# Performance work log

Measured on AMD Instinct MI355X. Metric: run time of the kernel, lower is better.

## Reference

```python
import jax, jax.numpy as jnp
import numpy as np

B, L, E, H = 1, 4096, 1024, 16
D = E // H
EPS = 1e-6


def setup_inputs() -> dict:
    key = jax.random.key(0)
    k1, k2, k3 = jax.random.split(key, 3)
    # fan-in scaled init to keep activations sane
    x = jax.random.normal(k1, (B, L, E), dtype=jnp.float32)
    qkv_w = jax.random.normal(k2, (E, 3 * E), dtype=jnp.float32) / np.sqrt(E)
    qkv_b = jnp.zeros((3 * E,), dtype=jnp.float32)
    out_w = jax.random.normal(k3, (E, E), dtype=jnp.float32) / np.sqrt(E)
    out_b = jnp.zeros((E,), dtype=jnp.float32)
    return {"x": x, "qkv_w": qkv_w, "qkv_b": qkv_b, "out_w": out_w, "out_b": out_b}


def reference(x, qkv_w, qkv_b, out_w, out_b):
    b, l, e = x.shape
    qkv = x @ qkv_w + qkv_b                      # (B, L, 3E)
    q, k, v = jnp.split(qkv, 3, axis=-1)
    # (B, L, E) -> (B, H, L, D)
    q = q.reshape(b, l, H, D).transpose(0, 2, 1, 3)
    k = k.reshape(b, l, H, D).transpose(0, 2, 1, 3)
    v = v.reshape(b, l, H, D).transpose(0, 2, 1, 3)
    q_prime = jax.nn.elu(q) + 1.0
    k_prime = jax.nn.elu(k) + 1.0
    # cumulative sum of per-position outer products k'_l v_l^T : (B,H,L,D,D)
    kv_prod = jnp.einsum('bhld,bhle->bhlde', k_prime, v)
    kv_cumsum = jnp.cumsum(kv_prod, axis=2)
    context = jnp.einsum('bhld,bhlde->bhle', q_prime, kv_cumsum)  # (B,H,L,D)
    k_cumsum = jnp.cumsum(k_prime, axis=2)                        # (B,H,L,D)
    norm = jnp.einsum('bhld,bhld->bhl', q_prime, k_cumsum)        # (B,H,L)
    output = context / (norm[..., None] + EPS)
    output = output.transpose(0, 2, 1, 3).reshape(b, l, e)
    return output @ out_w + out_b
```

## Files before the change

### kernel.cpp

```cpp
#include <hip/hip_runtime.h>
#include <cstddef>
#include <cstdint>

#define L_SEQ 4096
#define EMB   1024
#define NH    16
#define HD    64
#define N3    3072
#define CHUNK 64
#define NCHUNK 64
#define EPS 1e-6f

typedef __attribute__((ext_vector_type(8))) short   bf16x8;
typedef __attribute__((ext_vector_type(4))) short   bf16x4;
typedef __attribute__((ext_vector_type(4))) float   floatx4;

#define AS1 __attribute__((address_space(1)))
#define AS3 __attribute__((address_space(3)))

__device__ __forceinline__ void gload_lds16(const void* g, void* l) {
    __builtin_amdgcn_global_load_lds((AS1 const unsigned int*)g,
                                     (AS3 unsigned int*)l, 16, 0, 0);
}

__device__ __forceinline__ short f2bf(float f) {
    union { float f; unsigned u; } a; a.f = f;
    unsigned r = a.u + 0x7fffu + ((a.u >> 16) & 1u);
    return (short)(r >> 16);
}
__device__ __forceinline__ float bf2f(short s) {
    union { unsigned u; float f; } a; a.u = ((unsigned)(unsigned short)s) << 16;
    return a.f;
}

__device__ __forceinline__ void transpose_tile(const float* __restrict__ W,
                                               short* __restrict__ WT,
                                               int K, int N, int bx, int by,
                                               float (*t)[65], int tid)
{
    const int r  = tid >> 4;
    const int c4 = (tid & 15) << 2;
#pragma unroll
    for (int s = 0; s < 4; ++s) {
        const int k = r + s * 16;
        const floatx4 v = *(const floatx4*)&W[(size_t)(by * 64 + k) * N + bx * 64 + c4];
        t[k][c4 + 0] = v[0]; t[k][c4 + 1] = v[1];
        t[k][c4 + 2] = v[2]; t[k][c4 + 3] = v[3];
    }
    __syncthreads();
#pragma unroll
    for (int s = 0; s < 4; ++s) {
        const int n = r + s * 16;
        bf16x4 o;
        o[0] = f2bf(t[c4 + 0][n]); o[1] = f2bf(t[c4 + 1][n]);
        o[2] = f2bf(t[c4 + 2][n]); o[3] = f2bf(t[c4 + 3][n]);
        *(bf16x4*)&WT[(size_t)(bx * 64 + n) * K + by * 64 + c4] = o;
    }
}

__global__ __launch_bounds__(256)
void prep(const float* __restrict__ x, short* __restrict__ xb,
          const float* __restrict__ qkv_w, short* __restrict__ qwt,
          const float* __restrict__ out_w, short* __restrict__ owt)
{
    __shared__ float t[64][65];
    const int b = blockIdx.x;
    const int tid = threadIdx.x;
    if (b < 2048) {
        const int i = b * 256 + tid;
        const floatx4 a = *(const floatx4*)(x + (size_t)i * 8);
        const floatx4 c = *(const floatx4*)(x + (size_t)i * 8 + 4);
        bf16x8 o;
        o[0] = f2bf(a[0]); o[1] = f2bf(a[1]); o[2] = f2bf(a[2]); o[3] = f2bf(a[3]);
        o[4] = f2bf(c[0]); o[5] = f2bf(c[1]); o[6] = f2bf(c[2]); o[7] = f2bf(c[3]);
        *(bf16x8*)(xb + (size_t)i * 8) = o;
    } else if (b < 2048 + 768) {
        const int u = b - 2048;
        transpose_tile(qkv_w, qwt, EMB, N3, u % 48, u / 48, t, tid);
    } else {
        const int u = b - 2816;
        transpose_tile(out_w, owt, EMB, EMB, u & 15, u >> 4, t, tid);
    }
}

#define MFMA16 __builtin_amdgcn_mfma_f32_16x16x32_bf16

__global__ __launch_bounds__(512, 2)
void mfma_gemm_qkv256(const short* __restrict__ A, const short* __restrict__ BT,
                      const float* __restrict__ bias,
                      short* __restrict__ OQ, short* __restrict__ OK,
                      short* __restrict__ OV)
{
    __shared__ __align__(16) short lds[65536];
    const int tid  = threadIdx.x;
    const int lane = tid & 63;
    const int wave = tid >> 6;
    const int wr   = wave >> 2;
    const int wc   = wave & 3;
    const int frow = lane & 15;
    const int quad = lane >> 4;
    const int q8   = quad * 8;
    const int bx = blockIdx.x;
    const int by = blockIdx.y;

    const short* Ab = A  + (size_t)(by * 256) * 1024;
    const short* Bb = BT + (size_t)(bx * 256) * 1024;

    const int trow = tid >> 3;
    const int ccol = (tid & 7) * 8;
    const int scol = ccol ^ ((trow & 12) << 2);
    const int sx = (frow & 12) << 2;
    const int wcb = wc * 64 + frow;

#define STG(LBASE, GPTR) do {                                               \
        const short* g_ = (GPTR);                                           \
        _Pragma("unroll")                                                   \
        for (int j_ = 0; j_ < 2; ++j_) {                                    \
            const int r_ = j_ * 64 + trow;                                  \
            gload_lds16(g_ + (size_t)r_ * 1024 + scol,                      \
                        &lds[(LBASE) + r_ * 64 + ccol]);                    \
        }                                                                   \
    } while (0)

#define LDA(BASE, R, KS) \
    (*(const bf16x8*)&lds[(BASE) + (R) * 64 + ((((KS) * 32) + q8) ^ sx)])

    floatx4 acc[8][4] = {};
    bf16x8  bq[4][2];

#define PHASE(ABASE, BBASE, QD, RDB, VM, ...) do {                          \
        const int Rr_ = wr * 128 + (QD) * 32 + frow;                        \
        bf16x8 a0_ = LDA((ABASE), Rr_,      0);                             \
        bf16x8 a1_ = LDA((ABASE), Rr_,      1);                             \
        bf16x8 a2_ = LDA((ABASE), Rr_ + 16, 0);                             \
        bf16x8 a3_ = LDA((ABASE), Rr_ + 16, 1);                             \
        if (RDB) {                                                          \
            _Pragma("unroll")                                               \
            for (int ni_ = 0; ni_ < 4; ++ni_) {                             \
                bq[ni_][0] = LDA((BBASE), wcb + ni_ * 16, 0);               \
                bq[ni_][1] = LDA((BBASE), wcb + ni_ * 16, 1);               \
            }                                                               \
        }                                                                   \
        __VA_ARGS__;                                                        \
        __builtin_amdgcn_sched_barrier(0);                                  \
        __builtin_amdgcn_s_barrier();                                       \
        asm volatile("s_waitcnt lgkmcnt(0)" ::: "memory");                  \
        __builtin_amdgcn_sched_barrier(0);                                  \
        __builtin_amdgcn_s_setprio(1);                                      \
        _Pragma("unroll")                                                   \
        for (int ni_ = 0; ni_ < 4; ++ni_) {                                 \
            acc[2*(QD)  ][ni_] = MFMA16(a0_, bq[ni_][0], acc[2*(QD)  ][ni_], 0,0,0); \
            acc[2*(QD)  ][ni_] = MFMA16(a1_, bq[ni_][1], acc[2*(QD)  ][ni_], 0,0,0); \
            acc[2*(QD)+1][ni_] = MFMA16(a2_, bq[ni_][0], acc[2*(QD)+1][ni_], 0,0,0); \
            acc[2*(QD)+1][ni_] = MFMA16(a3_, bq[ni_][1], acc[2*(QD)+1][ni_], 0,0,0); \
        }                                                                   \
        __builtin_amdgcn_s_setprio(0);                                      \
        if (VM) asm volatile("s_waitcnt vmcnt(4)" ::: "memory");            \
        __builtin_amdgcn_s_barrier();                                       \
        __builtin_amdgcn_sched_barrier(0);                                  \
    } while (0)

    STG(0,     Ab);
    STG(8192,  Ab + 131072);
    STG(16384, Bb);
    STG(24576, Bb + 131072);
    STG(49152, Bb + 64);
    STG(57344, Bb + 131072 + 64);
    asm volatile("s_waitcnt vmcnt(4)" ::: "memory");
    __builtin_amdgcn_s_barrier();
    __builtin_amdgcn_sched_barrier(0);

#pragma unroll 1
    for (int it = 0; it < 8; ++it) {
        const int k1  = (2 * it + 1) * 64;
        const int kn0 = ((2 * it + 2) & 15) * 64;
        const int kn1 = ((2 * it + 3) & 15) * 64;

        PHASE(0, 16384, 0, 1, 0,
              STG(32768, Ab + k1); STG(40960, Ab + 131072 + k1));
        PHASE(0, 16384, 1, 0, 0, STG(16384, Bb + kn0));
        PHASE(0, 16384, 2, 0, 0, STG(24576, Bb + 131072 + kn0));
        PHASE(0, 16384, 3, 0, 1, ((void)0));
        PHASE(32768, 49152, 0, 1, 0, STG(0,    Ab + kn0));
        PHASE(32768, 49152, 1, 0, 0, STG(8192, Ab + 131072 + kn0));
        PHASE(32768, 49152, 2, 0, 0, STG(49152, Bb + kn1));
        PHASE(32768, 49152, 3, 0, 1, STG(57344, Bb + 131072 + kn1));
    }

    __syncthreads();

    const int wbase = wave * 8192;
    const int colg0 = bx * 256 + wc * 64;
    const int rsel  = colg0 >> 10;
    const bool do_elu = rsel < 2;
    short* obase = (rsel == 0) ? OQ : (rsel == 1 ? OK : OV);
    const int h  = (colg0 >> 6) & 15;
    const int L0 = by * 256 + wr * 128;
#pragma unroll
    for (int ni = 0; ni < 4; ++ni) {
        const float bv = bias[colg0 + ni * 16 + frow];
#pragma unroll
        for (int mi = 0; mi < 8; ++mi)
#pragma unroll
            for (int r = 0; r < 4; ++r) {
                float v = acc[mi][ni][r] + bv;
                if (do_elu) v = (v > 0.f) ? (v + 1.f) : __expf(v);
                lds[wbase + (mi * 16 + quad * 4 + r) * 64 + ni * 16 + frow] = f2bf(v);
            }
    }
#pragma unroll
    for (int s = 0; s < 16; ++s) {
        const int chunk = s * 64 + lane;
        const int row = chunk >> 3, c8 = (chunk & 7) * 8;
        *(bf16x8*)&obase[((size_t)(h * L_SEQ + L0 + row)) * HD + c8] =
            *(const bf16x8*)&lds[wbase + row * 64 + c8];
    }
#undef PHASE
#undef LDA
#undef STG
}

__global__ __launch_bounds__(256)
void mfma_gemm_out(const short* __restrict__ A, const short* __restrict__ BT,
                   const float* __restrict__ bias, float* __restrict__ OF,
                   int N, int K)
{
    __shared__ __align__(16) short smem[12288];
    short* pan[4] = { smem, smem + 2048, smem + 6144, smem + 8192 };
    const int tid  = threadIdx.x;
    const int lane = tid & 63;
    const int wave = tid >> 6;
    const int wm = (wave >> 1) * 32;
    const int wn = (wave & 1) * 64;
    const int bx = blockIdx.x;
    const int by = blockIdx.y;
    const int frow = lane & 15;
    const int quad = lane >> 4;
    const int fko  = quad << 3;

    const short* Ab = A  + (size_t)(by * 64) * K;
    const short* Bb = BT + (size_t)(bx * 128) * K;

    floatx4 acc[2][4] = {};

    for (int k0 = 0; k0 < K; k0 += 64) {
#pragma unroll
        for (int p = 0; p < 2; ++p) {
            const int kp = k0 + p * 32;
            {
                const int row = tid >> 2;
                const int kc  = (tid & 3) << 3;
                gload_lds16(Ab + (size_t)row * K + kp + kc, &pan[p * 2 + 0][tid << 3]);
            }
#pragma unroll
            for (int q = 0; q < 2; ++q) {
                const int ib = q * 256 + tid;
                const int row = ib >> 2;
                const int kc  = (ib & 3) << 3;
                gload_lds16(Bb + (size_t)row * K + kp + kc, &pan[p * 2 + 1][ib << 3]);
            }
        }
        __syncthreads();
#pragma unroll
        for (int p = 0; p < 2; ++p) {
            bf16x8 af[2], bfv[4];
#pragma unroll
            for (int mi = 0; mi < 2; ++mi)
                af[mi] = *(const bf16x8*)&pan[p * 2 + 0][(wm + mi * 16 + frow) * 32 + fko];
#pragma unroll
            for (int ni = 0; ni < 4; ++ni)
                bfv[ni] = *(const bf16x8*)&pan[p * 2 + 1][(wn + ni * 16 + frow) * 32 + fko];
#pragma unroll
            for (int mi = 0; mi < 2; ++mi)
#pragma unroll
                for (int ni = 0; ni < 4; ++ni)
                    acc[mi][ni] = __builtin_amdgcn_mfma_f32_16x16x32_bf16(
                        af[mi], bfv[ni], acc[mi][ni], 0, 0, 0);
        }
        __syncthreads();
    }

    const int rq = quad << 2;
#pragma unroll
    for (int ni = 0; ni < 4; ++ni) {
        const int n = bx * 128 + wn + ni * 16 + frow;
        const float bv = bias[n];
#pragma unroll
        for (int mi = 0; mi < 2; ++mi)
#pragma unroll
            for (int r = 0; r < 4; ++r) {
                const int m = by * 64 + wm + mi * 16 + rq + r;
                OF[(size_t)m * N + n] = acc[mi][ni][r] + bv;
            }
    }
}

#define SP 72

__global__ __launch_bounds__(256, 4)
void chunk_state(const short* __restrict__ Kb, const short* __restrict__ Vb,
                 short* __restrict__ ScTb, float* __restrict__ zc)
{
    __shared__ __align__(16) short Vt[64 * SP];
    __shared__ __align__(16) short Kt[64 * SP];
    const int c = blockIdx.x, h = blockIdx.y;
    const int tid = threadIdx.x, lane = tid & 63, wave = tid >> 6;
    const int frow = lane & 15;
    const int quad = lane >> 4;
    const int fko  = quad << 3;
    const int wm   = wave << 4;
    const short* Kg = Kb + ((size_t)h * L_SEQ + (size_t)c * CHUNK) * HD;
    const short* Vg = Vb + ((size_t)h * L_SEQ + (size_t)c * CHUNK) * HD;

#pragma unroll
    for (int q = 0; q < 2; ++q) {
        const int idx = q * 256 + tid;
        const int l = idx >> 3, c8 = (idx & 7) << 3;
        const bf16x8 vv = *(const bf16x8*)&Vg[l * 64 + c8];
        const bf16x8 kk = *(const bf16x8*)&Kg[l * 64 + c8];
#pragma unroll
        for (int j = 0; j < 8; ++j) {
            Vt[(c8 + j) * SP + l] = vv[j];
            Kt[(c8 + j) * SP + l] = kk[j];
        }
    }
    __syncthreads();

    const bf16x8 af0 = *(const bf16x8*)&Vt[(wm + frow) * SP + fko];
    const bf16x8 af1 = *(const bf16x8*)&Vt[(wm + frow) * SP + 32 + fko];

    floatx4 acc[4] = {};
#pragma unroll
    for (int n = 0; n < 4; ++n) {
        const bf16x8 kf0 = *(const bf16x8*)&Kt[(n * 16 + frow) * SP + fko];
        const bf16x8 kf1 = *(const bf16x8*)&Kt[(n * 16 + frow) * SP + 32 + fko];
        acc[n] = __builtin_amdgcn_mfma_f32_16x16x32_bf16(af0, kf0, acc[n], 0, 0, 0);
        acc[n] = __builtin_amdgcn_mfma_f32_16x16x32_bf16(af1, kf1, acc[n], 0, 0, 0);
    }

    short* Sout = ScTb + (size_t)(h * NCHUNK + c) * 4096;
#pragma unroll
    for (int n = 0; n < 4; ++n)
#pragma unroll
        for (int r = 0; r < 4; ++r) {
            const int e = wm + quad * 4 + r;
            const int d = n * 16 + frow;
            Sout[e * 64 + d] = f2bf(acc[n][r]);
        }

    if (wave == 0) {
        bf16x8 ones;
#pragma unroll
        for (int j = 0; j < 8; ++j) ones[j] = (short)0x3F80;
        floatx4 zacc[4] = {};
#pragma unroll
        for (int n = 0; n < 4; ++n) {
            const bf16x8 kf0 = *(const bf16x8*)&Kt[(n * 16 + frow) * SP + fko];
            const bf16x8 kf1 = *(const bf16x8*)&Kt[(n * 16 + frow) * SP + 32 + fko];
            zacc[n] = __builtin_amdgcn_mfma_f32_16x16x32_bf16(ones, kf0, zacc[n], 0, 0, 0);
            zacc[n] = __builtin_amdgcn_mfma_f32_16x16x32_bf16(ones, kf1, zacc[n], 0, 0, 0);
        }
        if (quad == 0) {
#pragma unroll
            for (int n = 0; n < 4; ++n)
                zc[(size_t)(h * NCHUNK + c) * 64 + n * 16 + frow] = zacc[n][0];
        }
    }
}

__global__ __launch_bounds__(256)
void prefix_scan(const short* __restrict__ ScTb, const float* __restrict__ zc,
                 short* __restrict__ S0b)
{
    const int g = blockIdx.x * 256 + threadIdx.x;
    const int h  = g >> 12;
    const int ed = g & 4095;
    const int e  = ed >> 6;
    const int d  = ed & 63;
    const short* src = ScTb + (size_t)h * NCHUNK * 4096 + ed;
    float run = 0.f;
    for (int cb = 0; cb < NCHUNK; cb += 8) {
        short v[8];
#pragma unroll
        for (int u = 0; u < 8; ++u) v[u] = src[(size_t)(cb + u) * 4096];
#pragma unroll
        for (int u = 0; u < 8; ++u) {
            S0b[((size_t)((h * NCHUNK + cb + u) * 65 + e)) * 64 + d] = f2bf(run);
            run += bf2f(v[u]);
        }
    }
    if (g < NH * HD) {
        const int h2 = g >> 6, d2 = g & 63;
        float rz = 0.f;
        for (int cb = 0; cb < NCHUNK; cb += 8) {
            float w[8];
#pragma unroll
            for (int u = 0; u < 8; ++u)
                w[u] = zc[((size_t)(h2 * NCHUNK + cb + u)) * HD + d2];
#pragma unroll
            for (int u = 0; u < 8; ++u) {
                S0b[((size_t)((h2 * NCHUNK + cb + u) * 65 + 64)) * 64 + d2] = f2bf(rz);
                rz += w[u];
            }
        }
    }
}

__global__ __launch_bounds__(256)
void chunk_attn(const short* __restrict__ Qb, const short* __restrict__ Kb,
                const short* __restrict__ Vb, const short* __restrict__ S0b,
                short* __restrict__ attn)
{
    __shared__ __align__(16) short Vs[65 * SP];
    __shared__ __align__(16) short As[64 * SP];
    const int c = blockIdx.x, h = blockIdx.y;
    const int tid = threadIdx.x, lane = tid & 63, wave = tid >> 6;
    const size_t rb = ((size_t)h * L_SEQ + (size_t)c * CHUNK) * HD;
    const short* Qg = Qb + rb;
    const short* Kg = Kb + rb;
    const short* Vg = Vb + rb;
    const short* Sg = S0b + (size_t)(h * NCHUNK + c) * 65 * 64;

#pragma unroll
    for (int q = 0; q < 2; ++q) {
        const int idx = q * 256 + tid;
        const int row = idx >> 3, c8 = (idx & 7) << 3;
        const bf16x8 vv = *(const bf16x8*)&Vg[row * 64 + c8];
#pragma unroll
        for (int j = 0; j < 8; ++j) Vs[(c8 + j) * SP + row] = vv[j];
    }
    if (tid < 64) Vs[64 * SP + tid] = (short)0x3F80;
    __syncthreads();

    const int frow = lane & 15;
    const int quad = lane >> 4;
    const int fko  = quad << 3;
    const int wm   = wave << 4;

    const bf16x8 qf0 = *(const bf16x8*)&Qg[(wm + frow) * 64 + fko];
    const bf16x8 qf1 = *(const bf16x8*)&Qg[(wm + frow) * 64 + 32 + fko];

    floatx4 sacc[4] = {};
#pragma unroll
    for (int n = 0; n < 4; ++n) {
        const bf16x8 kf0 = *(const bf16x8*)&Kg[(n * 16 + frow) * 64 + fko];
        const bf16x8 kf1 = *(const bf16x8*)&Kg[(n * 16 + frow) * 64 + 32 + fko];
        sacc[n] = __builtin_amdgcn_mfma_f32_16x16x32_bf16(qf0, kf0, sacc[n], 0, 0, 0);
        sacc[n] = __builtin_amdgcn_mfma_f32_16x16x32_bf16(qf1, kf1, sacc[n], 0, 0, 0);
    }
#pragma unroll
    for (int n = 0; n < 4; ++n)
#pragma unroll
        for (int r = 0; r < 4; ++r) {
            const int i = wm + quad * 4 + r;
            const int j = n * 16 + frow;
            As[i * SP + j] = (j <= i) ? f2bf(sacc[n][r]) : (short)0;
        }
    const bf16x8 af0 = *(const bf16x8*)&As[(wm + frow) * SP + fko];
    const bf16x8 af1 = *(const bf16x8*)&As[(wm + frow) * SP + 32 + fko];

    floatx4 oacc[5] = {};
#pragma unroll
    for (int n = 0; n < 4; ++n) {
        const bf16x8 vf0 = *(const bf16x8*)&Vs[(n * 16 + frow) * SP + fko];
        const bf16x8 vf1 = *(const bf16x8*)&Vs[(n * 16 + frow) * SP + 32 + fko];
        oacc[n] = __builtin_amdgcn_mfma_f32_16x16x32_bf16(af0, vf0, oacc[n], 0, 0, 0);
        oacc[n] = __builtin_amdgcn_mfma_f32_16x16x32_bf16(af1, vf1, oacc[n], 0, 0, 0);
        const bf16x8 sf0 = *(const bf16x8*)&Sg[(n * 16 + frow) * 64 + fko];
        const bf16x8 sf1 = *(const bf16x8*)&Sg[(n * 16 + frow) * 64 + 32 + fko];
        oacc[n] = __builtin_amdgcn_mfma_f32_16x16x32_bf16(qf0, sf0, oacc[n], 0, 0, 0);
        oacc[n] = __builtin_amdgcn_mfma_f32_16x16x32_bf16(qf1, sf1, oacc[n], 0, 0, 0);
    }
    {
        const bf16x8 vf0 = *(const bf16x8*)&Vs[64 * SP + fko];
        const bf16x8 vf1 = *(const bf16x8*)&Vs[64 * SP + 32 + fko];
        oacc[4] = __builtin_amdgcn_mfma_f32_16x16x32_bf16(af0, vf0, oacc[4], 0, 0, 0);
        oacc[4] = __builtin_amdgcn_mfma_f32_16x16x32_bf16(af1, vf1, oacc[4], 0, 0, 0);
        const bf16x8 sf0 = *(const bf16x8*)&Sg[64 * 64 + fko];
        const bf16x8 sf1 = *(const bf16x8*)&Sg[64 * 64 + 32 + fko];
        oacc[4] = __builtin_amdgcn_mfma_f32_16x16x32_bf16(qf0, sf0, oacc[4], 0, 0, 0);
        oacc[4] = __builtin_amdgcn_mfma_f32_16x16x32_bf16(qf1, sf1, oacc[4], 0, 0, 0);
    }
#pragma unroll
    for (int r = 0; r < 4; ++r) {
        const float norm = __shfl(oacc[4][r], lane & 48) + EPS;
        const float inv = 1.f / norm;
        const int i = wm + quad * 4 + r;
#pragma unroll
        for (int n = 0; n < 4; ++n)
            As[i * SP + n * 16 + frow] = f2bf(oacc[n][r] * inv);
    }
    __syncthreads();
#pragma unroll
    for (int t = 0; t < 2; ++t) {
        const int idx = t * 256 + tid;
        const int row = idx >> 3, c8 = (idx & 7) << 3;
        *(bf16x8*)&attn[(size_t)(c * CHUNK + row) * EMB + h * HD + c8] =
            *(const bf16x8*)&As[row * SP + c8];
    }
}

extern "C" void kernel_launch(void* const* d_in, const int* in_sizes, int n_in,
                              void* d_out, int out_size, void* d_ws, size_t ws_size,
                              hipStream_t stream)
{
    const float* x     = (const float*)d_in[0];
    const float* qkv_w = (const float*)d_in[1];
    const float* qkv_b = (const float*)d_in[2];
    const float* out_w = (const float*)d_in[3];
    const float* out_b = (const float*)d_in[4];
    float* out = (float*)d_out;

    short* ws    = (short*)d_ws;
    short* Qb    = ws;
    short* Kb    = Qb + 4194304;
    short* Vb    = Kb + 4194304;
    short* xb    = Vb + 4194304;
    short* qwt   = xb + 4194304;
    short* owt   = qwt + 3145728;
    short* attnb = owt + 1048576;
    short* ScTb  = attnb + 4194304;
    short* S0b   = ScTb + 4194304;
    float* zc    = (float*)(S0b + 4259840);

    prep<<<dim3(3072), 256, 0, stream>>>(x, xb, qkv_w, qwt, out_w, owt);
    mfma_gemm_qkv256<<<dim3(N3 / 256, L_SEQ / 256), 512, 0, stream>>>(
        xb, qwt, qkv_b, Qb, Kb, Vb);
    chunk_state<<<dim3(NCHUNK, NH), 256, 0, stream>>>(Kb, Vb, ScTb, zc);
    prefix_scan<<<dim3((NH * 4096) / 256), 256, 0, stream>>>(ScTb, zc, S0b);
    chunk_attn<<<dim3(NCHUNK, NH), 256, 0, stream>>>(Qb, Kb, Vb, S0b, attnb);
    mfma_gemm_out<<<dim3(EMB / 128, L_SEQ / 64), 256, 0, stream>>>(
        attnb, owt, out_b, out, EMB, EMB);
}
```

Baseline: 168.3 us.

## Fuse chunk state, prefix scan, chunk attention and output GEMM into one persistent kernel

```diff
diff --git a/kernel.cpp b/kernel.cpp
--- a/kernel.cpp
+++ b/kernel.cpp
@@ -33,6 +33,37 @@
     return a.f;
 }
 
+__device__ __forceinline__ void gbar(unsigned* bar, int tid, int grp)
+{
+    __syncthreads();
+    if (tid == 0) {
+        __builtin_amdgcn_fence(__ATOMIC_RELEASE, "agent");
+        unsigned* gen = bar + 17;
+        const unsigned g0 =
+            __hip_atomic_load(gen, __ATOMIC_RELAXED, __HIP_MEMORY_SCOPE_AGENT);
+        bool released = false;
+        if (__hip_atomic_fetch_add(bar + grp, 1u, __ATOMIC_RELAXED,
+                                   __HIP_MEMORY_SCOPE_AGENT) == 63u) {
+            __hip_atomic_store(bar + grp, 0u, __ATOMIC_RELAXED,
+                               __HIP_MEMORY_SCOPE_AGENT);
+            if (__hip_atomic_fetch_add(bar + 16, 1u, __ATOMIC_RELAXED,
+                                       __HIP_MEMORY_SCOPE_AGENT) == 15u) {
+                __hip_atomic_store(bar + 16, 0u, __ATOMIC_RELAXED,
+                                   __HIP_MEMORY_SCOPE_AGENT);
+                __hip_atomic_store(gen, g0 + 1u, __ATOMIC_RELEASE,
+                                   __HIP_MEMORY_SCOPE_AGENT);
+                released = true;
+            }
+        }
+        if (!released)
+            while (__hip_atomic_load(gen, __ATOMIC_RELAXED,
+                                     __HIP_MEMORY_SCOPE_AGENT) == g0)
+                __builtin_amdgcn_s_sleep(4);
+        __builtin_amdgcn_fence(__ATOMIC_ACQUIRE, "agent");
+    }
+    __syncthreads();
+}
+
 __device__ __forceinline__ void transpose_tile(const float* __restrict__ W,
                                                short* __restrict__ WT,
                                                int K, int N, int bx, int by,
@@ -61,11 +92,13 @@
 __global__ __launch_bounds__(256)
 void prep(const float* __restrict__ x, short* __restrict__ xb,
           const float* __restrict__ qkv_w, short* __restrict__ qwt,
-          const float* __restrict__ out_w, short* __restrict__ owt)
+          const float* __restrict__ out_w, short* __restrict__ owt,
+          unsigned* __restrict__ bar)
 {
     __shared__ float t[64][65];
     const int b = blockIdx.x;
     const int tid = threadIdx.x;
+    if (b == 0 && tid < 32) bar[tid] = 0u;
     if (b < 2048) {
         const int i = b * 256 + tid;
         const floatx4 a = *(const floatx4*)(x + (size_t)i * 8);
@@ -220,283 +253,274 @@
 #undef STG
 }
 
-__global__ __launch_bounds__(256)
-void mfma_gemm_out(const short* __restrict__ A, const short* __restrict__ BT,
-                   const float* __restrict__ bias, float* __restrict__ OF,
-                   int N, int K)
+#define SP 72
+
+__global__ __launch_bounds__(256, 4)
+void tail(const short* __restrict__ Qb, const short* __restrict__ Kb,
+          const short* __restrict__ Vb,
+          short* __restrict__ ScTb, float* __restrict__ zc,
+          short* __restrict__ S0b, short* __restrict__ attnb,
+          const short* __restrict__ owt, const float* __restrict__ out_b,
+          float* __restrict__ out, unsigned* __restrict__ bar)
 {
-    __shared__ __align__(16) short smem[12288];
-    short* pan[4] = { smem, smem + 2048, smem + 6144, smem + 8192 };
+    __shared__ __align__(16) short shm[12288];
     const int tid  = threadIdx.x;
     const int lane = tid & 63;
     const int wave = tid >> 6;
-    const int wm = (wave >> 1) * 32;
-    const int wn = (wave & 1) * 64;
-    const int bx = blockIdx.x;
-    const int by = blockIdx.y;
+    const int bidf = blockIdx.y * 64 + blockIdx.x;
     const int frow = lane & 15;
     const int quad = lane >> 4;
     const int fko  = quad << 3;
 
-    const short* Ab = A  + (size_t)(by * 64) * K;
-    const short* Bb = BT + (size_t)(bx * 128) * K;
-
-    floatx4 acc[2][4] = {};
-
-    for (int k0 = 0; k0 < K; k0 += 64) {
-#pragma unroll
-        for (int p = 0; p < 2; ++p) {
-            const int kp = k0 + p * 32;
-            {
-                const int row = tid >> 2;
-                const int kc  = (tid & 3) << 3;
-                gload_lds16(Ab + (size_t)row * K + kp + kc, &pan[p * 2 + 0][tid << 3]);
-            }
-#pragma unroll
-            for (int q = 0; q < 2; ++q) {
-                const int ib = q * 256 + tid;
-                const int row = ib >> 2;
-                const int kc  = (ib & 3) << 3;
-                gload_lds16(Bb + (size_t)row * K + kp + kc, &pan[p * 2 + 1][ib << 3]);
+    {
+        short* Vt = shm;
+        short* Kt = shm + 64 * SP;
+        const int c = blockIdx.x, h = blockIdx.y;
+        const int wm = wave << 4;
+        const short* Kg = Kb + ((size_t)h * L_SEQ + (size_t)c * CHUNK) * HD;
+        const short* Vg = Vb + ((size_t)h * L_SEQ + (size_t)c * CHUNK) * HD;
+
+#pragma unroll
+        for (int q = 0; q < 2; ++q) {
+            const int idx = q * 256 + tid;
+            const int l = idx >> 3, c8 = (idx & 7) << 3;
+            const bf16x8 vv = *(const bf16x8*)&Vg[l * 64 + c8];
+            const bf16x8 kk = *(const bf16x8*)&Kg[l * 64 + c8];
+#pragma unroll
+            for (int j = 0; j < 8; ++j) {
+                Vt[(c8 + j) * SP + l] = vv[j];
+                Kt[(c8 + j) * SP + l] = kk[j];
             }
         }
         __syncthreads();
-#pragma unroll
-        for (int p = 0; p < 2; ++p) {
-            bf16x8 af[2], bfv[4];
-#pragma unroll
-            for (int mi = 0; mi < 2; ++mi)
-                af[mi] = *(const bf16x8*)&pan[p * 2 + 0][(wm + mi * 16 + frow) * 32 + fko];
-#pragma unroll
-            for (int ni = 0; ni < 4; ++ni)
-                bfv[ni] = *(const bf16x8*)&pan[p * 2 + 1][(wn + ni * 16 + frow) * 32 + fko];
-#pragma unroll
-            for (int mi = 0; mi < 2; ++mi)
-#pragma unroll
-                for (int ni = 0; ni < 4; ++ni)
-                    acc[mi][ni] = __builtin_amdgcn_mfma_f32_16x16x32_bf16(
-                        af[mi], bfv[ni], acc[mi][ni], 0, 0, 0);
-        }
-        __syncthreads();
-    }
-
-    const int rq = quad << 2;
-#pragma unroll
-    for (int ni = 0; ni < 4; ++ni) {
-        const int n = bx * 128 + wn + ni * 16 + frow;
-        const float bv = bias[n];
-#pragma unroll
-        for (int mi = 0; mi < 2; ++mi)
-#pragma unroll
-            for (int r = 0; r < 4; ++r) {
-                const int m = by * 64 + wm + mi * 16 + rq + r;
-                OF[(size_t)m * N + n] = acc[mi][ni][r] + bv;
-            }
-    }
-}
-
-#define SP 72
-
-__global__ __launch_bounds__(256, 4)
-void chunk_state(const short* __restrict__ Kb, const short* __restrict__ Vb,
-                 short* __restrict__ ScTb, float* __restrict__ zc)
-{
-    __shared__ __align__(16) short Vt[64 * SP];
-    __shared__ __align__(16) short Kt[64 * SP];
-    const int c = blockIdx.x, h = blockIdx.y;
-    const int tid = threadIdx.x, lane = tid & 63, wave = tid >> 6;
-    const int frow = lane & 15;
-    const int quad = lane >> 4;
-    const int fko  = quad << 3;
-    const int wm   = wave << 4;
-    const short* Kg = Kb + ((size_t)h * L_SEQ + (size_t)c * CHUNK) * HD;
-    const short* Vg = Vb + ((size_t)h * L_SEQ + (size_t)c * CHUNK) * HD;
-
-#pragma unroll
-    for (int q = 0; q < 2; ++q) {
-        const int idx = q * 256 + tid;
-        const int l = idx >> 3, c8 = (idx & 7) << 3;
-        const bf16x8 vv = *(const bf16x8*)&Vg[l * 64 + c8];
-        const bf16x8 kk = *(const bf16x8*)&Kg[l * 64 + c8];
-#pragma unroll
-        for (int j = 0; j < 8; ++j) {
-            Vt[(c8 + j) * SP + l] = vv[j];
-            Kt[(c8 + j) * SP + l] = kk[j];
-        }
-    }
-    __syncthreads();
-
-    const bf16x8 af0 = *(const bf16x8*)&Vt[(wm + frow) * SP + fko];
-    const bf16x8 af1 = *(const bf16x8*)&Vt[(wm + frow) * SP + 32 + fko];
-
-    floatx4 acc[4] = {};
-#pragma unroll
-    for (int n = 0; n < 4; ++n) {
-        const bf16x8 kf0 = *(const bf16x8*)&Kt[(n * 16 + frow) * SP + fko];
-        const bf16x8 kf1 = *(const bf16x8*)&Kt[(n * 16 + frow) * SP + 32 + fko];
-        acc[n] = __builtin_amdgcn_mfma_f32_16x16x32_bf16(af0, kf0, acc[n], 0, 0, 0);
-        acc[n] = __builtin_amdgcn_mfma_f32_16x16x32_bf16(af1, kf1, acc[n], 0, 0, 0);
-    }
-
-    short* Sout = ScTb + (size_t)(h * NCHUNK + c) * 4096;
-#pragma unroll
-    for (int n = 0; n < 4; ++n)
-#pragma unroll
-        for (int r = 0; r < 4; ++r) {
-            const int e = wm + quad * 4 + r;
-            const int d = n * 16 + frow;
-            Sout[e * 64 + d] = f2bf(acc[n][r]);
-        }
-
-    if (wave == 0) {
-        bf16x8 ones;
-#pragma unroll
-        for (int j = 0; j < 8; ++j) ones[j] = (short)0x3F80;
-        floatx4 zacc[4] = {};
+
+        const bf16x8 af0 = *(const bf16x8*)&Vt[(wm + frow) * SP + fko];
+        const bf16x8 af1 = *(const bf16x8*)&Vt[(wm + frow) * SP + 32 + fko];
+
+        floatx4 acc[4] = {};
 #pragma unroll
         for (int n = 0; n < 4; ++n) {
             const bf16x8 kf0 = *(const bf16x8*)&Kt[(n * 16 + frow) * SP + fko];
             const bf16x8 kf1 = *(const bf16x8*)&Kt[(n * 16 + frow) * SP + 32 + fko];
-            zacc[n] = __builtin_amdgcn_mfma_f32_16x16x32_bf16(ones, kf0, zacc[n], 0, 0, 0);
-            zacc[n] = __builtin_amdgcn_mfma_f32_16x16x32_bf16(ones, kf1, zacc[n], 0, 0, 0);
-        }
-        if (quad == 0) {
+            acc[n] = MFMA16(af0, kf0, acc[n], 0, 0, 0);
+            acc[n] = MFMA16(af1, kf1, acc[n], 0, 0, 0);
+        }
+
+        short* Sout = ScTb + (size_t)(h * NCHUNK + c) * 4096;
+#pragma unroll
+        for (int n = 0; n < 4; ++n)
+#pragma unroll
+            for (int r = 0; r < 4; ++r) {
+                const int e = wm + quad * 4 + r;
+                const int d = n * 16 + frow;
+                Sout[e * 64 + d] = f2bf(acc[n][r]);
+            }
+
+        if (wave == 0) {
+            bf16x8 ones;
+#pragma unroll
+            for (int j = 0; j < 8; ++j) ones[j] = (short)0x3F80;
+            floatx4 zacc[4] = {};
+#pragma unroll
+            for (int n = 0; n < 4; ++n) {
+                const bf16x8 kf0 = *(const bf16x8*)&Kt[(n * 16 + frow) * SP + fko];
+                const bf16x8 kf1 = *(const bf16x8*)&Kt[(n * 16 + frow) * SP + 32 + fko];
+                zacc[n] = MFMA16(ones, kf0, zacc[n], 0, 0, 0);
+                zacc[n] = MFMA16(ones, kf1, zacc[n], 0, 0, 0);
+            }
+            if (quad == 0) {
+#pragma unroll
+                for (int n = 0; n < 4; ++n)
+                    zc[(size_t)(h * NCHUNK + c) * 64 + n * 16 + frow] = zacc[n][0];
+            }
+        }
+    }
+    gbar(bar, tid, blockIdx.y);
+
+    if (bidf < 256) {
+        const int g = bidf * 256 + tid;
+        const int h  = g >> 12;
+        const int ed = g & 4095;
+        const int e  = ed >> 6;
+        const int d  = ed & 63;
+        const short* src = ScTb + (size_t)h * NCHUNK * 4096 + ed;
+        float run = 0.f;
+        for (int cb = 0; cb < NCHUNK; cb += 8) {
+            short v[8];
+#pragma unroll
+            for (int u = 0; u < 8; ++u) v[u] = src[(size_t)(cb + u) * 4096];
+#pragma unroll
+            for (int u = 0; u < 8; ++u) {
+                S0b[((size_t)((h * NCHUNK + cb + u) * 65 + e)) * 64 + d] = f2bf(run);
+                run += bf2f(v[u]);
+            }
+        }
+        if (g < NH * HD) {
+            const int h2 = g >> 6, d2 = g & 63;
+            float rz = 0.f;
+            for (int cb = 0; cb < NCHUNK; cb += 8) {
+                float w[8];
+#pragma unroll
+                for (int u = 0; u < 8; ++u)
+                    w[u] = zc[((size_t)(h2 * NCHUNK + cb + u)) * HD + d2];
+#pragma unroll
+                for (int u = 0; u < 8; ++u) {
+                    S0b[((size_t)((h2 * NCHUNK + cb + u) * 65 + 64)) * 64 + d2] = f2bf(rz);
+                    rz += w[u];
+                }
+            }
+        }
+    }
+    gbar(bar, tid, blockIdx.y);
+
+    {
+        short* Vs = shm;
+        short* As = shm + 65 * SP;
+        const int c = blockIdx.x, h = blockIdx.y;
+        const int wm = wave << 4;
+        const size_t rb = ((size_t)h * L_SEQ + (size_t)c * CHUNK) * HD;
+        const short* Qg = Qb + rb;
+        const short* Kg = Kb + rb;
+        const short* Vg = Vb + rb;
+        const short* Sg = S0b + (size_t)(h * NCHUNK + c) * 65 * 64;
+
+#pragma unroll
+        for (int q = 0; q < 2; ++q) {
+            const int idx = q * 256 + tid;
+            const int row = idx >> 3, c8 = (idx & 7) << 3;
+            const bf16x8 vv = *(const bf16x8*)&Vg[row * 64 + c8];
+#pragma unroll
+            for (int j = 0; j < 8; ++j) Vs[(c8 + j) * SP + row] = vv[j];
+        }
+        if (tid < 64) Vs[64 * SP + tid] = (short)0x3F80;
+        __syncthreads();
+
+        const bf16x8 qf0 = *(const bf16x8*)&Qg[(wm + frow) * 64 + fko];
+        const bf16x8 qf1 = *(const bf16x8*)&Qg[(wm + frow) * 64 + 32 + fko];
+
+        floatx4 sacc[4] = {};
+#pragma unroll
+        for (int n = 0; n < 4; ++n) {
+            const bf16x8 kf0 = *(const bf16x8*)&Kg[(n * 16 + frow) * 64 + fko];
+            const bf16x8 kf1 = *(const bf16x8*)&Kg[(n * 16 + frow) * 64 + 32 + fko];
+            sacc[n] = MFMA16(qf0, kf0, sacc[n], 0, 0, 0);
+            sacc[n] = MFMA16(qf1, kf1, sacc[n], 0, 0, 0);
+        }
+#pragma unroll
+        for (int n = 0; n < 4; ++n)
+#pragma unroll
+            for (int r = 0; r < 4; ++r) {
+                const int i = wm + quad * 4 + r;
+                const int j = n * 16 + frow;
+                As[i * SP + j] = (j <= i) ? f2bf(sacc[n][r]) : (short)0;
+            }
+        const bf16x8 af0 = *(const bf16x8*)&As[(wm + frow) * SP + fko];
+        const bf16x8 af1 = *(const bf16x8*)&As[(wm + frow) * SP + 32 + fko];
+
+        floatx4 oacc[5] = {};
+#pragma unroll
+        for (int n = 0; n < 4; ++n) {
+            const bf16x8 vf0 = *(const bf16x8*)&Vs[(n * 16 + frow) * SP + fko];
+            const bf16x8 vf1 = *(const bf16x8*)&Vs[(n * 16 + frow) * SP + 32 + fko];
+            oacc[n] = MFMA16(af0, vf0, oacc[n], 0, 0, 0);
+            oacc[n] = MFMA16(af1, vf1, oacc[n], 0, 0, 0);
+            const bf16x8 sf0 = *(const bf16x8*)&Sg[(n * 16 + frow) * 64 + fko];
+            const bf16x8 sf1 = *(const bf16x8*)&Sg[(n * 16 + frow) * 64 + 32 + fko];
+            oacc[n] = MFMA16(qf0, sf0, oacc[n], 0, 0, 0);
+            oacc[n] = MFMA16(qf1, sf1, oacc[n], 0, 0, 0);
+        }
+        {
+            const bf16x8 vf0 = *(const bf16x8*)&Vs[64 * SP + fko];
+            const bf16x8 vf1 = *(const bf16x8*)&Vs[64 * SP + 32 + fko];
+            oacc[4] = MFMA16(af0, vf0, oacc[4], 0, 0, 0);
+            oacc[4] = MFMA16(af1, vf1, oacc[4], 0, 0, 0);
+            const bf16x8 sf0 = *(const bf16x8*)&Sg[64 * 64 + fko];
+            const bf16x8 sf1 = *(const bf16x8*)&Sg[64 * 64 + 32 + fko];
+            oacc[4] = MFMA16(qf0, sf0, oacc[4], 0, 0, 0);
+            oacc[4] = MFMA16(qf1, sf1, oacc[4], 0, 0, 0);
+        }
+#pragma unroll
+        for (int r = 0; r < 4; ++r) {
+            const float norm = __shfl(oacc[4][r], lane & 48) + EPS;
+            const float inv = 1.f / norm;
+            const int i = wm + quad * 4 + r;
 #pragma unroll
             for (int n = 0; n < 4; ++n)
-                zc[(size_t)(h * NCHUNK + c) * 64 + n * 16 + frow] = zacc[n][0];
-        }
-    }
-}
-
-__global__ __launch_bounds__(256)
-void prefix_scan(const short* __restrict__ ScTb, const float* __restrict__ zc,
-                 short* __restrict__ S0b)
-{
-    const int g = blockIdx.x * 256 + threadIdx.x;
-    const int h  = g >> 12;
-    const int ed = g & 4095;
-    const int e  = ed >> 6;
-    const int d  = ed & 63;
-    const short* src = ScTb + (size_t)h * NCHUNK * 4096 + ed;
-    float run = 0.f;
-    for (int cb = 0; cb < NCHUNK; cb += 8) {
-        short v[8];
-#pragma unroll
-        for (int u = 0; u < 8; ++u) v[u] = src[(size_t)(cb + u) * 4096];
-#pragma unroll
-        for (int u = 0; u < 8; ++u) {
-            S0b[((size_t)((h * NCHUNK + cb + u) * 65 + e)) * 64 + d] = f2bf(run);
-            run += bf2f(v[u]);
-        }
-    }
-    if (g < NH * HD) {
-        const int h2 = g >> 6, d2 = g & 63;
-        float rz = 0.f;
-        for (int cb = 0; cb < NCHUNK; cb += 8) {
-            float w[8];
-#pragma unroll
-            for (int u = 0; u < 8; ++u)
-                w[u] = zc[((size_t)(h2 * NCHUNK + cb + u)) * HD + d2];
-#pragma unroll
-            for (int u = 0; u < 8; ++u) {
-                S0b[((size_t)((h2 * NCHUNK + cb + u) * 65 + 64)) * 64 + d2] = f2bf(rz);
-                rz += w[u];
-            }
-        }
-    }
-}
-
-__global__ __launch_bounds__(256)
-void chunk_attn(const short* __restrict__ Qb, const short* __restrict__ Kb,
-                const short* __restrict__ Vb, const short* __restrict__ S0b,
-                short* __restrict__ attn)
-{
-    __shared__ __align__(16) short Vs[65 * SP];
-    __shared__ __align__(16) short As[64 * SP];
-    const int c = blockIdx.x, h = blockIdx.y;
-    const int tid = threadIdx.x, lane = tid & 63, wave = tid >> 6;
-    const size_t rb = ((size_t)h * L_SEQ + (size_t)c * CHUNK) * HD;
-    const short* Qg = Qb + rb;
-    const short* Kg = Kb + rb;
-    const short* Vg = Vb + rb;
-    const short* Sg = S0b + (size_t)(h * NCHUNK + c) * 65 * 64;
-
-#pragma unroll
-    for (int q = 0; q < 2; ++q) {
-        const int idx = q * 256 + tid;
-        const int row = idx >> 3, c8 = (idx & 7) << 3;
-        const bf16x8 vv = *(const bf16x8*)&Vg[row * 64 + c8];
-#pragma unroll
-        for (int j = 0; j < 8; ++j) Vs[(c8 + j) * SP + row] = vv[j];
-    }
-    if (tid < 64) Vs[64 * SP + tid] = (short)0x3F80;
-    __syncthreads();
-
-    const int frow = lane & 15;
-    const int quad = lane >> 4;
-    const int fko  = quad << 3;
-    const int wm   = wave << 4;
-
-    const bf16x8 qf0 = *(const bf16x8*)&Qg[(wm + frow) * 64 + fko];
-    const bf16x8 qf1 = *(const bf16x8*)&Qg[(wm + frow) * 64 + 32 + fko];
-
-    floatx4 sacc[4] = {};
-#pragma unroll
-    for (int n = 0; n < 4; ++n) {
-        const bf16x8 kf0 = *(const bf16x8*)&Kg[(n * 16 + frow) * 64 + fko];
-        const bf16x8 kf1 = *(const bf16x8*)&Kg[(n * 16 + frow) * 64 + 32 + fko];
-        sacc[n] = __builtin_amdgcn_mfma_f32_16x16x32_bf16(qf0, kf0, sacc[n], 0, 0, 0);
-        sacc[n] = __builtin_amdgcn_mfma_f32_16x16x32_bf16(qf1, kf1, sacc[n], 0, 0, 0);
-    }
-#pragma unroll
-    for (int n = 0; n < 4; ++n)
-#pragma unroll
-        for (int r = 0; r < 4; ++r) {
-            const int i = wm + quad * 4 + r;
-            const int j = n * 16 + frow;
-            As[i * SP + j] = (j <= i) ? f2bf(sacc[n][r]) : (short)0;
-        }
-    const bf16x8 af0 = *(const bf16x8*)&As[(wm + frow) * SP + fko];
-    const bf16x8 af1 = *(const bf16x8*)&As[(wm + frow) * SP + 32 + fko];
-
-    floatx4 oacc[5] = {};
-#pragma unroll
-    for (int n = 0; n < 4; ++n) {
-        const bf16x8 vf0 = *(const bf16x8*)&Vs[(n * 16 + frow) * SP + fko];
-        const bf16x8 vf1 = *(const bf16x8*)&Vs[(n * 16 + frow) * SP + 32 + fko];
-        oacc[n] = __builtin_amdgcn_mfma_f32_16x16x32_bf16(af0, vf0, oacc[n], 0, 0, 0);
-        oacc[n] = __builtin_amdgcn_mfma_f32_16x16x32_bf16(af1, vf1, oacc[n], 0, 0, 0);
-        const bf16x8 sf0 = *(const bf16x8*)&Sg[(n * 16 + frow) * 64 + fko];
-        const bf16x8 sf1 = *(const bf16x8*)&Sg[(n * 16 + frow) * 64 + 32 + fko];
-        oacc[n] = __builtin_amdgcn_mfma_f32_16x16x32_bf16(qf0, sf0, oacc[n], 0, 0, 0);
-        oacc[n] = __builtin_amdgcn_mfma_f32_16x16x32_bf16(qf1, sf1, oacc[n], 0, 0, 0);
-    }
-    {
-        const bf16x8 vf0 = *(const bf16x8*)&Vs[64 * SP + fko];
-        const bf16x8 vf1 = *(const bf16x8*)&Vs[64 * SP + 32 + fko];
-        oacc[4] = __builtin_amdgcn_mfma_f32_16x16x32_bf16(af0, vf0, oacc[4], 0, 0, 0);
-        oacc[4] = __builtin_amdgcn_mfma_f32_16x16x32_bf16(af1, vf1, oacc[4], 0, 0, 0);
-        const bf16x8 sf0 = *(const bf16x8*)&Sg[64 * 64 + fko];
-        const bf16x8 sf1 = *(const bf16x8*)&Sg[64 * 64 + 32 + fko];
-        oacc[4] = __builtin_amdgcn_mfma_f32_16x16x32_bf16(qf0, sf0, oacc[4], 0, 0, 0);
-        oacc[4] = __builtin_amdgcn_mfma_f32_16x16x32_bf16(qf1, sf1, oacc[4], 0, 0, 0);
-    }
-#pragma unroll
-    for (int r = 0; r < 4; ++r) {
-        const float norm = __shfl(oacc[4][r], lane & 48) + EPS;
-        const float inv = 1.f / norm;
-        const int i = wm + quad * 4 + r;
-#pragma unroll
-        for (int n = 0; n < 4; ++n)
-            As[i * SP + n * 16 + frow] = f2bf(oacc[n][r] * inv);
-    }
-    __syncthreads();
-#pragma unroll
-    for (int t = 0; t < 2; ++t) {
-        const int idx = t * 256 + tid;
-        const int row = idx >> 3, c8 = (idx & 7) << 3;
-        *(bf16x8*)&attn[(size_t)(c * CHUNK + row) * EMB + h * HD + c8] =
-            *(const bf16x8*)&As[row * SP + c8];
+                As[i * SP + n * 16 + frow] = f2bf(oacc[n][r] * inv);
+        }
+        __syncthreads();
+#pragma unroll
+        for (int t = 0; t < 2; ++t) {
+            const int idx = t * 256 + tid;
+            const int row = idx >> 3, c8 = (idx & 7) << 3;
+            *(bf16x8*)&attnb[(size_t)(c * CHUNK + row) * EMB + h * HD + c8] =
+                *(const bf16x8*)&As[row * SP + c8];
+        }
+    }
+    gbar(bar, tid, blockIdx.y);
+
+    if (bidf < 512) {
+        short* smem = shm;
+        short* pan[4] = { smem, smem + 2048, smem + 6144, smem + 8192 };
+        const int wm = (wave >> 1) * 32;
+        const int wn = (wave & 1) * 64;
+        const int bx = bidf & 7;
+        const int by = bidf >> 3;
+
+        const short* Ab = attnb + (size_t)(by * 64) * 1024;
+        const short* Bb = owt   + (size_t)(bx * 128) * 1024;
+
+        floatx4 acc[2][4] = {};
+
+        for (int k0 = 0; k0 < 1024; k0 += 64) {
+#pragma unroll
+            for (int p = 0; p < 2; ++p) {
+                const int kp = k0 + p * 32;
+                {
+                    const int row = tid >> 2;
+                    const int kc  = (tid & 3) << 3;
+                    gload_lds16(Ab + (size_t)row * 1024 + kp + kc, &pan[p * 2 + 0][tid << 3]);
+                }
+#pragma unroll
+                for (int q = 0; q < 2; ++q) {
+                    const int ib = q * 256 + tid;
+                    const int row = ib >> 2;
+                    const int kc  = (ib & 3) << 3;
+                    gload_lds16(Bb + (size_t)row * 1024 + kp + kc, &pan[p * 2 + 1][ib << 3]);
+                }
+            }
+            __syncthreads();
+#pragma unroll
+            for (int p = 0; p < 2; ++p) {
+                bf16x8 af[2], bfv[4];
+#pragma unroll
+                for (int mi = 0; mi < 2; ++mi)
+                    af[mi] = *(const bf16x8*)&pan[p * 2 + 0][(wm + mi * 16 + frow) * 32 + fko];
+#pragma unroll
+                for (int ni = 0; ni < 4; ++ni)
+                    bfv[ni] = *(const bf16x8*)&pan[p * 2 + 1][(wn + ni * 16 + frow) * 32 + fko];
+#pragma unroll
+                for (int mi = 0; mi < 2; ++mi)
+#pragma unroll
+                    for (int ni = 0; ni < 4; ++ni)
+                        acc[mi][ni] = MFMA16(af[mi], bfv[ni], acc[mi][ni], 0, 0, 0);
+            }
+            __syncthreads();
+        }
+
+        const int rq = quad << 2;
+#pragma unroll
+        for (int ni = 0; ni < 4; ++ni) {
+            const int n = bx * 128 + wn + ni * 16 + frow;
+            const float bv = out_b[n];
+#pragma unroll
+            for (int mi = 0; mi < 2; ++mi)
+#pragma unroll
+                for (int r = 0; r < 4; ++r) {
+                    const int m = by * 64 + wm + mi * 16 + rq + r;
+                    out[(size_t)m * 1024 + n] = acc[mi][ni][r] + bv;
+                }
+        }
     }
 }
 
@@ -522,13 +546,11 @@
     short* ScTb  = attnb + 4194304;
     short* S0b   = ScTb + 4194304;
     float* zc    = (float*)(S0b + 4259840);
-
-    prep<<<dim3(3072), 256, 0, stream>>>(x, xb, qkv_w, qwt, out_w, owt);
+    unsigned* bar = (unsigned*)(zc + 65536);
+
+    prep<<<dim3(3072), 256, 0, stream>>>(x, xb, qkv_w, qwt, out_w, owt, bar);
     mfma_gemm_qkv256<<<dim3(N3 / 256, L_SEQ / 256), 512, 0, stream>>>(
         xb, qwt, qkv_b, Qb, Kb, Vb);
-    chunk_state<<<dim3(NCHUNK, NH), 256, 0, stream>>>(Kb, Vb, ScTb, zc);
-    prefix_scan<<<dim3((NH * 4096) / 256), 256, 0, stream>>>(ScTb, zc, S0b);
-    chunk_attn<<<dim3(NCHUNK, NH), 256, 0, stream>>>(Qb, Kb, Vb, S0b, attnb);
-    mfma_gemm_out<<<dim3(EMB / 128, L_SEQ / 64), 256, 0, stream>>>(
-        attnb, owt, out_b, out, EMB, EMB);
-}
+    tail<<<dim3(NCHUNK, NH), 256, 0, stream>>>(
+        Qb, Kb, Vb, ScTb, zc, S0b, attnb, owt, out_b, out, bar);
+}
```

Result: slower. 429.9 us (+155.4%).
